# Kernel tuning notes

Hardware: AMD Instinct MI355X
Metric: run time of the kernel (lower is better)

Reference implementation:

```python
import jax, jax.numpy as jnp
import numpy as np

T, D, H, E, TOP_K = 8192, 1024, 4096, 8, 2


def setup_inputs() -> dict:
    key = jax.random.key(0)
    ks = jax.random.split(key, 4)
    s_in = 1.0 / np.sqrt(D)
    s_hid = 1.0 / np.sqrt(H)
    return {
        "x": jax.random.normal(ks[0], (T, D), dtype=jnp.float32),
        "Wg": jax.random.normal(ks[1], (D, E), dtype=jnp.float32) * s_in,
        "W1": jax.random.normal(ks[2], (E, D, H), dtype=jnp.float32) * s_in,
        "b1": jnp.zeros((E, H), dtype=jnp.float32),
        "W2": jax.random.normal(ks[3], (E, H, D), dtype=jnp.float32) * s_hid,
        "b2": jnp.zeros((E, D), dtype=jnp.float32),
    }


def _moe_forward(x, Wg, W1, b1, W2, b2):
    # Gating: router logits -> top-k -> renormalized softmax over selected experts
    logits = x @ Wg                                   # [T, E]
    top_vals, top_idx = jax.lax.top_k(logits, TOP_K)  # [T, K]
    gates = jax.nn.softmax(top_vals, axis=-1)         # [T, K]
    # Dense [T, E] combine weights (zero for unselected experts)
    w = jnp.zeros_like(logits).at[jnp.arange(x.shape[0])[:, None], top_idx].set(gates)
    # Per-expert 2-layer MLP computed densely, combined by gate weights
    h = jax.nn.relu(jnp.einsum("td,edh->teh", x, W1) + b1[None])   # [T, E, H]
    y = jnp.einsum("teh,ehd->ted", h, W2) + b2[None]               # [T, E, D]
    return jnp.einsum("te,ted->td", w, y)                          # [T, D]


def reference(x, Wg, W1, b1, W2, b2):
    # Deterministic main path of OuroborosMoELayer.forward: the topology-gated
    # domain shift fires only on a rare scalar condition; standard path is the
    # top-k MoE dispatch/combine.
    return _moe_forward(x, Wg, W1, b1, W2, b2)
```

## Files before the change

kernel.cpp:

```cpp
#include <hip/hip_runtime.h>
#include <hip/hip_bf16.h>

#define TT 8192
#define DD 1024
#define HH 4096
#define EE 8

typedef unsigned short u16;
typedef unsigned int u32;
typedef float fx4 __attribute__((ext_vector_type(4)));
typedef short s8v __attribute__((ext_vector_type(8)));
typedef int i4v __attribute__((ext_vector_type(4)));
typedef u16 u16x4 __attribute__((ext_vector_type(4)));

__device__ __forceinline__ u16 f2bf(float x) {
  union { float f; u32 u; } c; c.f = x;
  u32 r = (c.u + 0x7FFFu + ((c.u >> 16) & 1u)) >> 16;
  return (u16)r;
}

__device__ __forceinline__ void gl2lds16(const void* g, void* l) {
  __builtin_amdgcn_global_load_lds(
      (const __attribute__((address_space(1))) void*)g,
      (__attribute__((address_space(3))) void*)l, 16, 0, 0);
}

__global__ void zero_meta(int* counts) {
  if (threadIdx.x < EE) counts[threadIdx.x] = 0;
}

template<int R, int C>
__global__ void transpose_convert(const float* __restrict__ W, u16* __restrict__ Wt) {
  __shared__ float tile[64][65];
  const int e = blockIdx.z;
  const float* We = W + (size_t)e * R * C;
  u16* Wte = Wt + (size_t)e * R * C;
  const int r0 = blockIdx.y * 64, c0 = blockIdx.x * 64;
  const int tid = threadIdx.x;
  const int a = tid >> 4, b4 = (tid & 15) * 4;
#pragma unroll
  for (int i = 0; i < 4; ++i) {
    int rr = a + i * 16;
    float4 v = *(const float4*)(We + (size_t)(r0 + rr) * C + c0 + b4);
    tile[rr][b4 + 0] = v.x; tile[rr][b4 + 1] = v.y;
    tile[rr][b4 + 2] = v.z; tile[rr][b4 + 3] = v.w;
  }
  __syncthreads();
#pragma unroll
  for (int i = 0; i < 4; ++i) {
    int cc = a + i * 16;
    u16x4 o;
    o[0] = f2bf(tile[b4 + 0][cc]);
    o[1] = f2bf(tile[b4 + 1][cc]);
    o[2] = f2bf(tile[b4 + 2][cc]);
    o[3] = f2bf(tile[b4 + 3][cc]);
    *(u16x4*)(Wte + (size_t)(c0 + cc) * R + r0 + b4) = o;
  }
}

__global__ void router_kernel(const float* __restrict__ x, const float* __restrict__ Wg,
                              int* __restrict__ topIdx, float* __restrict__ gates,
                              int* __restrict__ counts, u16* __restrict__ xb) {
  __shared__ float wg[EE][DD + 1];
  const int tid = threadIdx.x;
  for (int i = tid; i < DD * EE; i += 256) wg[i & 7][i >> 3] = Wg[i];
  __syncthreads();
  const int w = tid >> 6, lane = tid & 63;
  const int t = blockIdx.x * 4 + w;
  double acc[EE];
#pragma unroll
  for (int e = 0; e < EE; ++e) acc[e] = 0.0;
  const float* xr = x + (size_t)t * DD;
  u16* xbr = xb + (size_t)t * DD;
  for (int i = 0; i < DD / 64; ++i) {
    int d = i * 64 + lane;
    float xf = xr[d];
    xbr[d] = f2bf(xf);
    double xv = (double)xf;
#pragma unroll
    for (int e = 0; e < EE; ++e) acc[e] += xv * (double)wg[e][d];
  }
#pragma unroll
  for (int e = 0; e < EE; ++e) {
    double v = acc[e];
#pragma unroll
    for (int s = 32; s > 0; s >>= 1) v += __shfl_xor(v, s, 64);
    acc[e] = v;
  }
  if (lane == 0) {
    float v0 = -3.4e38f, v1 = -3.4e38f; int i0 = 0, i1 = 0;
#pragma unroll
    for (int e = 0; e < EE; ++e) {
      float v = (float)acc[e];
      if (v > v0) { v1 = v0; i1 = i0; v0 = v; i0 = e; }
      else if (v > v1) { v1 = v; i1 = e; }
    }
    float ee = expf(v1 - v0);
    float g0 = 1.f / (1.f + ee);
    float g1 = ee / (1.f + ee);
    topIdx[t * 2 + 0] = i0; topIdx[t * 2 + 1] = i1;
    gates[t * 2 + 0] = g0; gates[t * 2 + 1] = g1;
    atomicAdd(&counts[i0], 1);
    atomicAdd(&counts[i1], 1);
  }
}

__global__ void prefix_kernel(const int* __restrict__ counts, int* __restrict__ offsets) {
  if (threadIdx.x == 0) {
    int s = 0;
    for (int e = 0; e < EE; ++e) { offsets[e] = s; s += counts[e]; }
    offsets[EE] = s;
  }
}

__global__ void scatter_det(const int* __restrict__ topIdx, const float* __restrict__ gates,
                            const int* __restrict__ offsets, int* __restrict__ entryTok,
                            float* __restrict__ entryGate) {
  const int e = blockIdx.x;
  const int tid = threadIdx.x;
  const int lane = tid & 63, w = tid >> 6;
  __shared__ int base;
  __shared__ int wsum[16];
  __shared__ int woff[16];
  __shared__ int chunktot;
  if (tid == 0) base = offsets[e];
  __syncthreads();
  for (int t0 = 0; t0 < TT; t0 += 1024) {
    int t = t0 + tid;
    int k = -1;
    if (topIdx[t * 2 + 0] == e) k = 0;
    else if (topIdx[t * 2 + 1] == e) k = 1;
    unsigned long long m = __ballot(k >= 0);
    int pre = __popcll(m & ((1ULL << lane) - 1ULL));
    if (lane == 0) wsum[w] = __popcll(m);
    __syncthreads();
    if (tid == 0) {
      int s = 0;
      for (int i = 0; i < 16; ++i) { woff[i] = s; s += wsum[i]; }
      chunktot = s;
    }
    __syncthreads();
    if (k >= 0) {
      int p = base + woff[w] + pre;
      entryTok[p] = t;
      entryGate[p] = gates[t * 2 + k];
    }
    __syncthreads();
    if (tid == 0) base += chunktot;
    __syncthreads();
  }
}

template<int K, int N>
__global__ __launch_bounds__(512) void moe_gemm1(
    const u16* __restrict__ A, const u16* __restrict__ Bt,
    const float* __restrict__ bias,
    const int* __restrict__ counts, const int* __restrict__ offsets,
    const int* __restrict__ entryTok, u16* __restrict__ hout) {
  constexpr int NM = TT / 128;
  constexpr int NX = N / 256;
  constexpr int nwg = EE * NX * NM;

  const int p = blockIdx.x;
  const int l = (p & 7) * (nwg >> 3) + (p >> 3);
  const int e = l / (NX * NM);
  const int lr = l % (NX * NM);
  const int nx = lr / NM;
  const int my = lr % NM;

  const int cnt = counts[e];
  const int mbase = my * 128;
  if (mbase >= cnt) return;
  const int off = offsets[e];
  const int nbase = nx * 256;
  const int tid = threadIdx.x;
  const int w = tid >> 6, lane = tid & 63;

  __shared__ __align__(16) u16 Asm[128][64];
  __shared__ __align__(16) u16 Bsm[256][64];

  const u16* asrc[2];
  const u16* bsrc[4];
  u32 adst[2], bdst[4];
#pragma unroll
  for (int j = 0; j < 2; ++j) {
    int c = j * 512 + tid;
    int row = c >> 3;
    int col = ((c & 7) ^ (row & 7)) * 8;
    int gm = mbase + row;
    int mm = (gm < cnt) ? gm : (cnt - 1);
    asrc[j] = A + (size_t)entryTok[off + mm] * K + col;
    adst[j] = (u32)c * 16;
  }
#pragma unroll
  for (int j = 0; j < 4; ++j) {
    int c = j * 512 + tid;
    int row = c >> 3;
    int col = ((c & 7) ^ (row & 7)) * 8;
    bsrc[j] = Bt + (size_t)e * N * K + (size_t)(nbase + row) * K + col;
    bdst[j] = (u32)c * 16;
  }

  const int wm = (w >> 2) * 64, wn = (w & 3) * 64;
  const int fl = lane & 15, fh = lane >> 4;
  const int fswz = fl & 7;

  fx4 acc[4][4];
#pragma unroll
  for (int mi = 0; mi < 4; ++mi)
#pragma unroll
    for (int ni = 0; ni < 4; ++ni)
      acc[mi][ni] = (fx4){0.f, 0.f, 0.f, 0.f};

  for (int kt = 0; kt < K; kt += 64) {
#pragma unroll
    for (int j = 0; j < 2; ++j)
      gl2lds16(asrc[j] + kt, (char*)&Asm[0][0] + adst[j]);
#pragma unroll
    for (int j = 0; j < 4; ++j)
      gl2lds16(bsrc[j] + kt, (char*)&Bsm[0][0] + bdst[j]);
    __syncthreads();
#pragma unroll
    for (int ks = 0; ks < 2; ++ks) {
      const int slot = ((ks * 4 + fh) ^ fswz) * 8;
      s8v af[4], bf[4];
#pragma unroll
      for (int i = 0; i < 4; ++i)
        af[i] = *(const s8v*)&Asm[wm + i * 16 + fl][slot];
#pragma unroll
      for (int i = 0; i < 4; ++i)
        bf[i] = *(const s8v*)&Bsm[wn + i * 16 + fl][slot];
#pragma unroll
      for (int mi = 0; mi < 4; ++mi)
#pragma unroll
        for (int ni = 0; ni < 4; ++ni)
          acc[mi][ni] = __builtin_amdgcn_mfma_f32_16x16x32_bf16(af[mi], bf[ni], acc[mi][ni], 0, 0, 0);
    }
    __syncthreads();
  }

#pragma unroll
  for (int mi = 0; mi < 4; ++mi) {
#pragma unroll
    for (int b = 0; b < 4; ++b) {
      int tm = wm + mi * 16 + fh * 4 + b;
      int gm = mbase + tm;
      if (gm < cnt) {
        u16* hrow = hout + (size_t)(off + gm) * N;
#pragma unroll
        for (int ni = 0; ni < 4; ++ni) {
          int n = nbase + wn + ni * 16 + fl;
          float v = acc[mi][ni][b] + bias[e * N + n];
          v = v > 0.f ? v : 0.f;
          hrow[n] = f2bf(v);
        }
      }
    }
  }
}

template<int K, int N>
__global__ __launch_bounds__(512) void moe_gemm2(
    const u16* __restrict__ A, const u16* __restrict__ Bt,
    const float* __restrict__ bias,
    const int* __restrict__ counts, const int* __restrict__ offsets,
    const int* __restrict__ entryTok, const float* __restrict__ entryGate,
    float* __restrict__ out) {
  constexpr int NM = TT / 256;
  constexpr int NX = N / 128;
  constexpr int nwg = EE * NX * NM;

  const int p = blockIdx.x;
  const int l = (p & 7) * (nwg >> 3) + (p >> 3);
  const int e = l / (NX * NM);
  const int lr = l % (NX * NM);
  const int nx = lr / NM;
  const int my = lr % NM;

  const int cnt = counts[e];
  const int mbase = my * 256;
  if (mbase >= cnt) return;
  const int off = offsets[e];
  const int nbase = nx * 128;
  const int tid = threadIdx.x;
  const int w = tid >> 6, lane = tid & 63;

  __shared__ __align__(16) u16 Asm[256][64];
  __shared__ __align__(16) u16 Bsm[128][64];

  const u16* asrc[4];
  const u16* bsrc[2];
  u32 adst[4], bdst[2];
#pragma unroll
  for (int j = 0; j < 4; ++j) {
    int c = j * 512 + tid;
    int row = c >> 3;
    int col = ((c & 7) ^ (row & 7)) * 8;
    int gm = mbase + row;
    int mm = (gm < cnt) ? gm : (cnt - 1);
    asrc[j] = A + (size_t)(off + mm) * K + col;
    adst[j] = (u32)c * 16;
  }
#pragma unroll
  for (int j = 0; j < 2; ++j) {
    int c = j * 512 + tid;
    int row = c >> 3;
    int col = ((c & 7) ^ (row & 7)) * 8;
    bsrc[j] = Bt + (size_t)e * N * K + (size_t)(nbase + row) * K + col;
    bdst[j] = (u32)c * 16;
  }

  const int wm = (w >> 1) * 64, wn = (w & 1) * 64;
  const int fl = lane & 15, fh = lane >> 4;
  const int fswz = fl & 7;

  fx4 acc[4][4];
#pragma unroll
  for (int mi = 0; mi < 4; ++mi)
#pragma unroll
    for (int ni = 0; ni < 4; ++ni)
      acc[mi][ni] = (fx4){0.f, 0.f, 0.f, 0.f};

  for (int kt = 0; kt < K; kt += 64) {
#pragma unroll
    for (int j = 0; j < 4; ++j)
      gl2lds16(asrc[j] + kt, (char*)&Asm[0][0] + adst[j]);
#pragma unroll
    for (int j = 0; j < 2; ++j)
      gl2lds16(bsrc[j] + kt, (char*)&Bsm[0][0] + bdst[j]);
    __syncthreads();
#pragma unroll
    for (int ks = 0; ks < 2; ++ks) {
      const int slot = ((ks * 4 + fh) ^ fswz) * 8;
      s8v af[4], bf[4];
#pragma unroll
      for (int i = 0; i < 4; ++i)
        af[i] = *(const s8v*)&Asm[wm + i * 16 + fl][slot];
#pragma unroll
      for (int i = 0; i < 4; ++i)
        bf[i] = *(const s8v*)&Bsm[wn + i * 16 + fl][slot];
#pragma unroll
      for (int mi = 0; mi < 4; ++mi)
#pragma unroll
        for (int ni = 0; ni < 4; ++ni)
          acc[mi][ni] = __builtin_amdgcn_mfma_f32_16x16x32_bf16(af[mi], bf[ni], acc[mi][ni], 0, 0, 0);
    }
    __syncthreads();
  }

#pragma unroll
  for (int mi = 0; mi < 4; ++mi) {
#pragma unroll
    for (int b = 0; b < 4; ++b) {
      int tm = wm + mi * 16 + fh * 4 + b;
      int gm = mbase + tm;
      if (gm < cnt) {
        int tok = entryTok[off + gm];
        float gate = entryGate[off + gm];
        float* orow = out + (size_t)tok * N;
#pragma unroll
        for (int ni = 0; ni < 4; ++ni) {
          int n = nbase + wn + ni * 16 + fl;
          float v = acc[mi][ni][b] + bias[e * N + n];
          atomicAdd(&orow[n], v * gate);
        }
      }
    }
  }
}

template<int EPI, int K, int N>
__global__ __launch_bounds__(256) void moe_gemm_slow(
    const u16* __restrict__ A, const float* __restrict__ Bw,
    const float* __restrict__ bias,
    const int* __restrict__ counts, const int* __restrict__ offsets,
    const int* __restrict__ entryTok, const float* __restrict__ entryGate,
    u16* __restrict__ hout, float* __restrict__ out) {
  const int e = blockIdx.z;
  const int cnt = counts[e];
  const int mbase = blockIdx.y * 128;
  if (mbase >= cnt) return;
  const int off = offsets[e];
  const int nbase = blockIdx.x * 128;
  const int tid = threadIdx.x;

  __shared__ u16 Asm[128][72];
  __shared__ u16 Bsm[128][72];
  __shared__ int rowTok[128];
  __shared__ float rowGate[128];

  if (tid < 128) {
    int m = mbase + tid;
    int valid = (m < cnt) ? 1 : 0;
    rowTok[tid] = valid ? entryTok[off + m] : -1;
    rowGate[tid] = valid ? entryGate[off + m] : 0.f;
  }
  __syncthreads();

  const int r = tid >> 1, half = tid & 1;
  const u16* arow;
  if (EPI == 0) {
    int tk = rowTok[r];
    arow = (tk >= 0) ? (A + (size_t)tk * K) : (const u16*)0;
  } else {
    int m = mbase + r;
    arow = (m < cnt) ? (A + (size_t)(off + m) * K) : (const u16*)0;
  }
  const int bk = tid >> 2;
  const int bn0 = (tid & 3) * 32;
  const float* bsrc = Bw + (size_t)e * K * N + (size_t)bk * N + nbase + bn0;

  const int w = tid >> 6, lane = tid & 63;
  const int wm = (w >> 1) * 64, wn = (w & 1) * 64;
  const int fl = lane & 15, fh = lane >> 4;

  fx4 acc[4][4];
#pragma unroll
  for (int mi = 0; mi < 4; ++mi)
#pragma unroll
    for (int ni = 0; ni < 4; ++ni)
      acc[mi][ni] = (fx4){0.f, 0.f, 0.f, 0.f};

  for (int kt = 0; kt < K; kt += 64) {
#pragma unroll
    for (int j = 0; j < 4; ++j) {
      int col = half * 32 + j * 8;
      i4v va = arow ? *(const i4v*)(arow + kt + col) : (i4v){0, 0, 0, 0};
      *(i4v*)&Asm[r][col] = va;
    }
#pragma unroll
    for (int j = 0; j < 8; ++j) {
      float4 v = *(const float4*)(bsrc + (size_t)kt * N + j * 4);
      Bsm[bn0 + j * 4 + 0][bk] = f2bf(v.x);
      Bsm[bn0 + j * 4 + 1][bk] = f2bf(v.y);
      Bsm[bn0 + j * 4 + 2][bk] = f2bf(v.z);
      Bsm[bn0 + j * 4 + 3][bk] = f2bf(v.w);
    }
    __syncthreads();
#pragma unroll
    for (int ks = 0; ks < 2; ++ks) {
      s8v af[4], bf[4];
#pragma unroll
      for (int i = 0; i < 4; ++i)
        af[i] = *(const s8v*)&Asm[wm + i * 16 + fl][ks * 32 + fh * 8];
#pragma unroll
      for (int i = 0; i < 4; ++i)
        bf[i] = *(const s8v*)&Bsm[wn + i * 16 + fl][ks * 32 + fh * 8];
#pragma unroll
      for (int mi = 0; mi < 4; ++mi)
#pragma unroll
        for (int ni = 0; ni < 4; ++ni)
          acc[mi][ni] = __builtin_amdgcn_mfma_f32_16x16x32_bf16(af[mi], bf[ni], acc[mi][ni], 0, 0, 0);
    }
    __syncthreads();
  }

#pragma unroll
  for (int mi = 0; mi < 4; ++mi) {
#pragma unroll
    for (int ni = 0; ni < 4; ++ni) {
      int n = nbase + wn + ni * 16 + fl;
      float bv = bias[e * N + n];
#pragma unroll
      for (int b = 0; b < 4; ++b) {
        int tm = wm + mi * 16 + fh * 4 + b;
        int gm = mbase + tm;
        if (gm < cnt) {
          float v = acc[mi][ni][b] + bv;
          if (EPI == 0) {
            v = v > 0.f ? v : 0.f;
            hout[(size_t)(off + gm) * N + n] = f2bf(v);
          } else {
            atomicAdd(&out[(size_t)rowTok[tm] * N + n], v * rowGate[tm]);
          }
        }
      }
    }
  }
}

extern "C" void kernel_launch(void* const* d_in, const int* in_sizes, int n_in,
                              void* d_out, int out_size, void* d_ws, size_t ws_size,
                              hipStream_t stream) {
  const float* x  = (const float*)d_in[0];
  const float* Wg = (const float*)d_in[1];
  const float* W1 = (const float*)d_in[2];
  const float* b1 = (const float*)d_in[3];
  const float* W2 = (const float*)d_in[4];
  const float* b2 = (const float*)d_in[5];
  float* out = (float*)d_out;

  char* ws = (char*)d_ws;
  int* counts  = (int*)(ws + 0);
  int* offsets = (int*)(ws + 128);
  size_t o = 256;
  int* topIdx = (int*)(ws + o);        o += (size_t)2 * TT * 4;
  float* gates = (float*)(ws + o);     o += (size_t)2 * TT * 4;
  int* entryTok = (int*)(ws + o);      o += (size_t)2 * TT * 4;
  float* entryGate = (float*)(ws + o); o += (size_t)2 * TT * 4;
  u16* xb  = (u16*)(ws + o);           o += (size_t)TT * DD * 2;

  const size_t FAST_REQ = (size_t)218366208;
  const bool fast = (ws_size >= FAST_REQ);

  hipMemsetAsync(d_out, 0, (size_t)TT * DD * 4, stream);
  zero_meta<<<1, 64, 0, stream>>>(counts);
  router_kernel<<<TT / 4, 256, 0, stream>>>(x, Wg, topIdx, gates, counts, xb);
  prefix_kernel<<<1, 1, 0, stream>>>(counts, offsets);
  scatter_det<<<EE, 1024, 0, stream>>>(topIdx, gates, offsets, entryTok, entryGate);

  if (fast) {
    u16* wbuf = (u16*)(ws + o);
    u16* hbuf = (u16*)(ws + o + (size_t)EE * DD * HH * 2);
    transpose_convert<DD, HH><<<dim3(HH / 64, DD / 64, EE), 256, 0, stream>>>(W1, wbuf);
    moe_gemm1<DD, HH><<<EE * (HH / 256) * (TT / 128), 512, 0, stream>>>(
        xb, wbuf, b1, counts, offsets, entryTok, hbuf);
    transpose_convert<HH, DD><<<dim3(DD / 64, HH / 64, EE), 256, 0, stream>>>(W2, wbuf);
    moe_gemm2<HH, DD><<<EE * (DD / 128) * (TT / 256), 512, 0, stream>>>(
        hbuf, wbuf, b2, counts, offsets, entryTok, entryGate, out);
  } else {
    u16* hbuf = (u16*)(ws + o);
    moe_gemm_slow<0, DD, HH><<<dim3(HH / 128, TT / 128, EE), 256, 0, stream>>>(
        xb, W1, b1, counts, offsets, entryTok, entryGate, hbuf, nullptr);
    moe_gemm_slow<1, HH, DD><<<dim3(DD / 128, TT / 128, EE), 256, 0, stream>>>(
        hbuf, W2, b2, counts, offsets, entryTok, entryGate, nullptr, out);
  }
}
```

Baseline: 728.6 us.

## Split-K second expert GEMM and replace ordered scatter with atomic cursor scatter

```diff
diff --git a/kernel.cpp b/kernel.cpp
--- a/kernel.cpp
+++ b/kernel.cpp
@@ -105,49 +105,25 @@
   }
 }
 
-__global__ void prefix_kernel(const int* __restrict__ counts, int* __restrict__ offsets) {
+__global__ void prefix_kernel(const int* __restrict__ counts, int* __restrict__ offsets,
+                              int* __restrict__ cursor) {
   if (threadIdx.x == 0) {
     int s = 0;
-    for (int e = 0; e < EE; ++e) { offsets[e] = s; s += counts[e]; }
+    for (int e = 0; e < EE; ++e) { offsets[e] = s; cursor[e] = s; s += counts[e]; }
     offsets[EE] = s;
   }
 }
 
-__global__ void scatter_det(const int* __restrict__ topIdx, const float* __restrict__ gates,
-                            const int* __restrict__ offsets, int* __restrict__ entryTok,
-                            float* __restrict__ entryGate) {
-  const int e = blockIdx.x;
-  const int tid = threadIdx.x;
-  const int lane = tid & 63, w = tid >> 6;
-  __shared__ int base;
-  __shared__ int wsum[16];
-  __shared__ int woff[16];
-  __shared__ int chunktot;
-  if (tid == 0) base = offsets[e];
-  __syncthreads();
-  for (int t0 = 0; t0 < TT; t0 += 1024) {
-    int t = t0 + tid;
-    int k = -1;
-    if (topIdx[t * 2 + 0] == e) k = 0;
-    else if (topIdx[t * 2 + 1] == e) k = 1;
-    unsigned long long m = __ballot(k >= 0);
-    int pre = __popcll(m & ((1ULL << lane) - 1ULL));
-    if (lane == 0) wsum[w] = __popcll(m);
-    __syncthreads();
-    if (tid == 0) {
-      int s = 0;
-      for (int i = 0; i < 16; ++i) { woff[i] = s; s += wsum[i]; }
-      chunktot = s;
-    }
-    __syncthreads();
-    if (k >= 0) {
-      int p = base + woff[w] + pre;
-      entryTok[p] = t;
-      entryGate[p] = gates[t * 2 + k];
-    }
-    __syncthreads();
-    if (tid == 0) base += chunktot;
-    __syncthreads();
+__global__ void scatter_atomic(const int* __restrict__ topIdx, const float* __restrict__ gates,
+                               int* __restrict__ cursor, int* __restrict__ entryTok,
+                               float* __restrict__ entryGate) {
+  int t = blockIdx.x * 256 + threadIdx.x;
+#pragma unroll
+  for (int k = 0; k < 2; ++k) {
+    int e = topIdx[t * 2 + k];
+    int p = atomicAdd(&cursor[e], 1);
+    entryTok[p] = t;
+    entryGate[p] = gates[t * 2 + k];
   }
 }
 
@@ -259,29 +235,32 @@
   }
 }
 
-template<int K, int N>
+template<int K, int N, int KSPLIT>
 __global__ __launch_bounds__(512) void moe_gemm2(
     const u16* __restrict__ A, const u16* __restrict__ Bt,
     const float* __restrict__ bias,
     const int* __restrict__ counts, const int* __restrict__ offsets,
     const int* __restrict__ entryTok, const float* __restrict__ entryGate,
     float* __restrict__ out) {
+  constexpr int KLEN = K / KSPLIT;
   constexpr int NM = TT / 256;
   constexpr int NX = N / 128;
-  constexpr int nwg = EE * NX * NM;
+  constexpr int nwg = EE * NX * NM * KSPLIT;
 
   const int p = blockIdx.x;
   const int l = (p & 7) * (nwg >> 3) + (p >> 3);
-  const int e = l / (NX * NM);
-  const int lr = l % (NX * NM);
-  const int nx = lr / NM;
-  const int my = lr % NM;
+  const int kh = l % KSPLIT;
+  int r = l / KSPLIT;
+  const int my = r % NM; r /= NM;
+  const int nx = r % NX;
+  const int e = r / NX;
 
   const int cnt = counts[e];
   const int mbase = my * 256;
   if (mbase >= cnt) return;
   const int off = offsets[e];
   const int nbase = nx * 128;
+  const int k0 = kh * KLEN;
   const int tid = threadIdx.x;
   const int w = tid >> 6, lane = tid & 63;
 
@@ -298,7 +277,7 @@
     int col = ((c & 7) ^ (row & 7)) * 8;
     int gm = mbase + row;
     int mm = (gm < cnt) ? gm : (cnt - 1);
-    asrc[j] = A + (size_t)(off + mm) * K + col;
+    asrc[j] = A + (size_t)(off + mm) * K + k0 + col;
     adst[j] = (u32)c * 16;
   }
 #pragma unroll
@@ -306,7 +285,7 @@
     int c = j * 512 + tid;
     int row = c >> 3;
     int col = ((c & 7) ^ (row & 7)) * 8;
-    bsrc[j] = Bt + (size_t)e * N * K + (size_t)(nbase + row) * K + col;
+    bsrc[j] = Bt + (size_t)e * N * K + (size_t)(nbase + row) * K + k0 + col;
     bdst[j] = (u32)c * 16;
   }
 
@@ -321,7 +300,7 @@
     for (int ni = 0; ni < 4; ++ni)
       acc[mi][ni] = (fx4){0.f, 0.f, 0.f, 0.f};
 
-  for (int kt = 0; kt < K; kt += 64) {
+  for (int kt = 0; kt < KLEN; kt += 64) {
 #pragma unroll
     for (int j = 0; j < 4; ++j)
       gl2lds16(asrc[j] + kt, (char*)&Asm[0][0] + adst[j]);
@@ -361,7 +340,7 @@
 #pragma unroll
         for (int ni = 0; ni < 4; ++ni) {
           int n = nbase + wn + ni * 16 + fl;
-          float v = acc[mi][ni][b] + bias[e * N + n];
+          float v = acc[mi][ni][b] + (kh == 0 ? bias[e * N + n] : 0.f);
           atomicAdd(&orow[n], v * gate);
         }
       }
@@ -492,6 +471,7 @@
 
   char* ws = (char*)d_ws;
   int* counts  = (int*)(ws + 0);
+  int* cursor  = (int*)(ws + 64);
   int* offsets = (int*)(ws + 128);
   size_t o = 256;
   int* topIdx = (int*)(ws + o);        o += (size_t)2 * TT * 4;
@@ -506,8 +486,8 @@
   hipMemsetAsync(d_out, 0, (size_t)TT * DD * 4, stream);
   zero_meta<<<1, 64, 0, stream>>>(counts);
   router_kernel<<<TT / 4, 256, 0, stream>>>(x, Wg, topIdx, gates, counts, xb);
-  prefix_kernel<<<1, 1, 0, stream>>>(counts, offsets);
-  scatter_det<<<EE, 1024, 0, stream>>>(topIdx, gates, offsets, entryTok, entryGate);
+  prefix_kernel<<<1, 1, 0, stream>>>(counts, offsets, cursor);
+  scatter_atomic<<<TT / 256, 256, 0, stream>>>(topIdx, gates, cursor, entryTok, entryGate);
 
   if (fast) {
     u16* wbuf = (u16*)(ws + o);
@@ -516,7 +496,7 @@
     moe_gemm1<DD, HH><<<EE * (HH / 256) * (TT / 128), 512, 0, stream>>>(
         xb, wbuf, b1, counts, offsets, entryTok, hbuf);
     transpose_convert<HH, DD><<<dim3(DD / 64, HH / 64, EE), 256, 0, stream>>>(W2, wbuf);
-    moe_gemm2<HH, DD><<<EE * (DD / 128) * (TT / 256), 512, 0, stream>>>(
+    moe_gemm2<HH, DD, 2><<<EE * (DD / 128) * (TT / 256) * 2, 512, 0, stream>>>(
         hbuf, wbuf, b2, counts, offsets, entryTok, entryGate, out);
   } else {
     u16* hbuf = (u16*)(ws + o);
```

Measured after the change: 784.7 us. 1.08x slower.

## Enlarge GEMM tiles to 256x256 with 1024 threads and split-K the second GEMM

Applied to the files above, without the earlier changes.

```diff
diff --git a/kernel.cpp b/kernel.cpp
--- a/kernel.cpp
+++ b/kernel.cpp
@@ -152,12 +152,12 @@
 }
 
 template<int K, int N>
-__global__ __launch_bounds__(512) void moe_gemm1(
+__global__ __launch_bounds__(1024) void moe_gemm1(
     const u16* __restrict__ A, const u16* __restrict__ Bt,
     const float* __restrict__ bias,
     const int* __restrict__ counts, const int* __restrict__ offsets,
     const int* __restrict__ entryTok, u16* __restrict__ hout) {
-  constexpr int NM = TT / 128;
+  constexpr int NM = TT / 256;
   constexpr int NX = N / 256;
   constexpr int nwg = EE * NX * NM;
 
@@ -169,34 +169,28 @@
   const int my = lr % NM;
 
   const int cnt = counts[e];
-  const int mbase = my * 128;
+  const int mbase = my * 256;
   if (mbase >= cnt) return;
   const int off = offsets[e];
   const int nbase = nx * 256;
   const int tid = threadIdx.x;
   const int w = tid >> 6, lane = tid & 63;
 
-  __shared__ __align__(16) u16 Asm[128][64];
+  __shared__ __align__(16) u16 Asm[256][64];
   __shared__ __align__(16) u16 Bsm[256][64];
 
   const u16* asrc[2];
-  const u16* bsrc[4];
-  u32 adst[2], bdst[4];
+  const u16* bsrc[2];
+  u32 adst[2], bdst[2];
 #pragma unroll
   for (int j = 0; j < 2; ++j) {
-    int c = j * 512 + tid;
+    int c = j * 1024 + tid;
     int row = c >> 3;
     int col = ((c & 7) ^ (row & 7)) * 8;
     int gm = mbase + row;
     int mm = (gm < cnt) ? gm : (cnt - 1);
     asrc[j] = A + (size_t)entryTok[off + mm] * K + col;
     adst[j] = (u32)c * 16;
-  }
-#pragma unroll
-  for (int j = 0; j < 4; ++j) {
-    int c = j * 512 + tid;
-    int row = c >> 3;
-    int col = ((c & 7) ^ (row & 7)) * 8;
     bsrc[j] = Bt + (size_t)e * N * K + (size_t)(nbase + row) * K + col;
     bdst[j] = (u32)c * 16;
   }
@@ -214,11 +208,10 @@
 
   for (int kt = 0; kt < K; kt += 64) {
 #pragma unroll
-    for (int j = 0; j < 2; ++j)
+    for (int j = 0; j < 2; ++j) {
       gl2lds16(asrc[j] + kt, (char*)&Asm[0][0] + adst[j]);
-#pragma unroll
-    for (int j = 0; j < 4; ++j)
       gl2lds16(bsrc[j] + kt, (char*)&Bsm[0][0] + bdst[j]);
+    }
     __syncthreads();
 #pragma unroll
     for (int ks = 0; ks < 2; ++ks) {
@@ -259,58 +252,55 @@
   }
 }
 
-template<int K, int N>
-__global__ __launch_bounds__(512) void moe_gemm2(
+template<int K, int N, int KSPLIT>
+__global__ __launch_bounds__(1024) void moe_gemm2(
     const u16* __restrict__ A, const u16* __restrict__ Bt,
     const float* __restrict__ bias,
     const int* __restrict__ counts, const int* __restrict__ offsets,
     const int* __restrict__ entryTok, const float* __restrict__ entryGate,
     float* __restrict__ out) {
+  constexpr int KLEN = K / KSPLIT;
   constexpr int NM = TT / 256;
-  constexpr int NX = N / 128;
-  constexpr int nwg = EE * NX * NM;
+  constexpr int NX = N / 256;
+  constexpr int nwg = EE * NX * NM * KSPLIT;
 
   const int p = blockIdx.x;
   const int l = (p & 7) * (nwg >> 3) + (p >> 3);
-  const int e = l / (NX * NM);
-  const int lr = l % (NX * NM);
-  const int nx = lr / NM;
-  const int my = lr % NM;
+  const int kh = l % KSPLIT;
+  int r = l / KSPLIT;
+  const int my = r % NM; r /= NM;
+  const int nx = r % NX;
+  const int e = r / NX;
 
   const int cnt = counts[e];
   const int mbase = my * 256;
   if (mbase >= cnt) return;
   const int off = offsets[e];
-  const int nbase = nx * 128;
+  const int nbase = nx * 256;
+  const int k0 = kh * KLEN;
   const int tid = threadIdx.x;
   const int w = tid >> 6, lane = tid & 63;
 
   __shared__ __align__(16) u16 Asm[256][64];
-  __shared__ __align__(16) u16 Bsm[128][64];
-
-  const u16* asrc[4];
+  __shared__ __align__(16) u16 Bsm[256][64];
+
+  const u16* asrc[2];
   const u16* bsrc[2];
-  u32 adst[4], bdst[2];
-#pragma unroll
-  for (int j = 0; j < 4; ++j) {
-    int c = j * 512 + tid;
+  u32 adst[2], bdst[2];
+#pragma unroll
+  for (int j = 0; j < 2; ++j) {
+    int c = j * 1024 + tid;
     int row = c >> 3;
     int col = ((c & 7) ^ (row & 7)) * 8;
     int gm = mbase + row;
     int mm = (gm < cnt) ? gm : (cnt - 1);
-    asrc[j] = A + (size_t)(off + mm) * K + col;
+    asrc[j] = A + (size_t)(off + mm) * K + k0 + col;
     adst[j] = (u32)c * 16;
-  }
-#pragma unroll
-  for (int j = 0; j < 2; ++j) {
-    int c = j * 512 + tid;
-    int row = c >> 3;
-    int col = ((c & 7) ^ (row & 7)) * 8;
-    bsrc[j] = Bt + (size_t)e * N * K + (size_t)(nbase + row) * K + col;
+    bsrc[j] = Bt + (size_t)e * N * K + (size_t)(nbase + row) * K + k0 + col;
     bdst[j] = (u32)c * 16;
   }
 
-  const int wm = (w >> 1) * 64, wn = (w & 1) * 64;
+  const int wm = (w >> 2) * 64, wn = (w & 3) * 64;
   const int fl = lane & 15, fh = lane >> 4;
   const int fswz = fl & 7;
 
@@ -321,13 +311,12 @@
     for (int ni = 0; ni < 4; ++ni)
       acc[mi][ni] = (fx4){0.f, 0.f, 0.f, 0.f};
 
-  for (int kt = 0; kt < K; kt += 64) {
-#pragma unroll
-    for (int j = 0; j < 4; ++j)
+  for (int kt = 0; kt < KLEN; kt += 64) {
+#pragma unroll
+    for (int j = 0; j < 2; ++j) {
       gl2lds16(asrc[j] + kt, (char*)&Asm[0][0] + adst[j]);
-#pragma unroll
-    for (int j = 0; j < 2; ++j)
       gl2lds16(bsrc[j] + kt, (char*)&Bsm[0][0] + bdst[j]);
+    }
     __syncthreads();
 #pragma unroll
     for (int ks = 0; ks < 2; ++ks) {
@@ -361,7 +350,7 @@
 #pragma unroll
         for (int ni = 0; ni < 4; ++ni) {
           int n = nbase + wn + ni * 16 + fl;
-          float v = acc[mi][ni][b] + bias[e * N + n];
+          float v = acc[mi][ni][b] + (kh == 0 ? bias[e * N + n] : 0.f);
           atomicAdd(&orow[n], v * gate);
         }
       }
@@ -513,10 +502,10 @@
     u16* wbuf = (u16*)(ws + o);
     u16* hbuf = (u16*)(ws + o + (size_t)EE * DD * HH * 2);
     transpose_convert<DD, HH><<<dim3(HH / 64, DD / 64, EE), 256, 0, stream>>>(W1, wbuf);
-    moe_gemm1<DD, HH><<<EE * (HH / 256) * (TT / 128), 512, 0, stream>>>(
+    moe_gemm1<DD, HH><<<EE * (HH / 256) * (TT / 256), 1024, 0, stream>>>(
         xb, wbuf, b1, counts, offsets, entryTok, hbuf);
     transpose_convert<HH, DD><<<dim3(DD / 64, HH / 64, EE), 256, 0, stream>>>(W2, wbuf);
-    moe_gemm2<HH, DD><<<EE * (DD / 128) * (TT / 256), 512, 0, stream>>>(
+    moe_gemm2<HH, DD, 2><<<EE * (DD / 256) * (TT / 256) * 2, 1024, 0, stream>>>(
         hbuf, wbuf, b2, counts, offsets, entryTok, entryGate, out);
   } else {
     u16* hbuf = (u16*)(ws + o);
```

After: 825.2 us. +13.3%, slower.
